# Kernel optimization log

Measured on AMD Instinct MI355X. Metric: run time of the kernel, lower is better.

Reference implementation:

```python
import jax, jax.numpy as jnp
import numpy as np

B, T1, CHUNK = 4, 512, 64
LEFT, RIGHT = 256, 64
T2 = T1 + LEFT + RIGHT          # 832
NPOS = 2 * T1 - 1 + LEFT + RIGHT  # 1343
NFEAT, H, DK = 1024, 16, 64


def setup_inputs() -> dict:
    key = jax.random.key(0)
    ks = jax.random.split(key, 14)
    s = 0.02
    inp = {
        "query":   jax.random.normal(ks[0], (B, T1, NFEAT), jnp.float32),
        "key":     jax.random.normal(ks[1], (B, T2, NFEAT), jnp.float32),
        "value":   jax.random.normal(ks[2], (B, T2, NFEAT), jnp.float32),
        "pos_emb": jax.random.normal(ks[3], (1, NPOS, NFEAT), jnp.float32),
        "Wq":   jax.random.normal(ks[4], (NFEAT, NFEAT), jnp.float32) * s,
        "bq":   jax.random.normal(ks[5], (NFEAT,), jnp.float32) * s,
        "Wk":   jax.random.normal(ks[6], (NFEAT, NFEAT), jnp.float32) * s,
        "bk":   jax.random.normal(ks[7], (NFEAT,), jnp.float32) * s,
        "Wv":   jax.random.normal(ks[8], (NFEAT, NFEAT), jnp.float32) * s,
        "bv":   jax.random.normal(ks[9], (NFEAT,), jnp.float32) * s,
        "Wpos": jax.random.normal(ks[10], (NFEAT, NFEAT), jnp.float32) * s,
        "Wout": jax.random.normal(ks[11], (NFEAT, NFEAT), jnp.float32) * s,
        "bout": jax.random.normal(ks[12], (NFEAT,), jnp.float32) * s,
        "pos_bias_u": jax.random.normal(ks[13], (H, DK), jnp.float32) * s,
        "pos_bias_v": jax.random.normal(jax.random.fold_in(key, 99), (H, DK), jnp.float32) * s,
    }
    # chunk mask with right context: key index j maps to absolute position a = j - LEFT;
    # query i (chunk c = i // CHUNK) may attend a in [c*CHUNK - LEFT, (c+1)*CHUNK + RIGHT)
    c = np.arange(T1) // CHUNK
    a = np.arange(T2) - LEFT
    allowed = (a[None, :] < (c[:, None] + 1) * CHUNK + RIGHT) & (a[None, :] >= c[:, None] * CHUNK - LEFT)
    inp["mask"] = jnp.broadcast_to(jnp.asarray(allowed, dtype=bool)[None], (B, T1, T2))
    inp["left_context_size"] = LEFT
    inp["right_context_size"] = RIGHT
    return inp


def _rel_shift(x, left, right):
    # x: (b, h, t1, 2*t1-1+left+right) -> (b, h, t1, t1+left+right)
    # matches torch as_strided: out[..., i, j] = x[..., i, j - i + t1 - 1]
    b, h, t1, n = x.shape
    t2 = t1 + left + right
    idx = jnp.arange(t2)[None, :] - jnp.arange(t1)[:, None] + (t1 - 1)  # (t1, t2)
    return jnp.take_along_axis(x, idx[None, None], axis=-1)


def reference(query, key, value, pos_emb, mask, Wq, bq, Wk, bk, Wv, bv,
              Wpos, Wout, bout, pos_bias_u, pos_bias_v,
              left_context_size, right_context_size):
    b, t1, _ = query.shape
    q = (query @ Wq.T + bq).reshape(b, t1, H, DK)                       # (b, t1, h, d)
    k = (key @ Wk.T + bk).reshape(b, -1, H, DK).transpose(0, 2, 1, 3)    # (b, h, t2, d)
    v = (value @ Wv.T + bv).reshape(b, -1, H, DK).transpose(0, 2, 1, 3)  # (b, h, t2, d)
    p = (pos_emb @ Wpos.T).reshape(pos_emb.shape[0], -1, H, DK).transpose(0, 2, 1, 3)  # (1, h, n, d)

    q_u = (q + pos_bias_u).transpose(0, 2, 1, 3)   # (b, h, t1, d)
    q_v = (q + pos_bias_v).transpose(0, 2, 1, 3)   # (b, h, t1, d)

    matrix_ac = jnp.einsum('bhqd,bhkd->bhqk', q_u, k)          # (b, h, t1, t2)
    matrix_bd = jnp.einsum('bhqd,ohnd->bhqn', q_v, p)          # (b, h, t1, n)
    matrix_bd = _rel_shift(matrix_bd, left_context_size, right_context_size)

    scores = (matrix_ac + matrix_bd) / jnp.sqrt(jnp.float32(DK))
    m = mask[:, None, :, :]                                    # (b, 1, t1, t2), True = attend
    scores = jnp.where(m, scores, -jnp.inf)
    attn = jax.nn.softmax(scores.astype(jnp.float32), axis=-1).astype(value.dtype)
    attn = jnp.where(m, attn, 0.0)

    x = jnp.einsum('bhqk,bhkd->bqhd', attn, v).reshape(b, t1, H * DK)
    out = x @ Wout.T + bout                                     # (b, t1, n_feat)
    new_cache = jnp.concatenate([k, v], axis=-1)                # (b, h, t2, 2*d)
    return out, new_cache
```

## Files before the change

kernel.cpp:

```cpp
#include <hip/hip_runtime.h>
#include <cstdint>

typedef unsigned short u16;
using short8 = __attribute__((ext_vector_type(8))) short;
using f32x4  = __attribute__((ext_vector_type(4))) float;

#define T1 512
#define T2 832
#define NH 16
#define NPLOC 448

__device__ __forceinline__ u16 f2b(float f){
  union { float f; uint32_t u; } c; c.f = f;
  uint32_t u = c.u;
  u += 0x7fffu + ((u >> 16) & 1u);
  return (u16)(u >> 16);
}
__device__ __forceinline__ float b2f(u16 b){
  union { uint32_t u; float f; } c; c.u = (uint32_t)b << 16; return c.f;
}
__device__ __forceinline__ void async16(const void* g, void* l){
  __builtin_amdgcn_global_load_lds(
      (const __attribute__((address_space(1))) unsigned int*)g,
      (__attribute__((address_space(3))) unsigned int*)l, 16, 0, 0);
}

struct CvtSeg { const float* src; u16* dst; int nblk; };
struct CvtArgs { CvtSeg s[9]; };

__global__ __launch_bounds__(256) void cvt_all(CvtArgs a){
  int rel = blockIdx.x, seg = 0;
  while (rel >= a.s[seg].nblk){ rel -= a.s[seg].nblk; ++seg; }
  int i = rel * 256 + threadIdx.x;
  float4 v = ((const float4*)a.s[seg].src)[i];
  uint64_t p = (uint64_t)f2b(v.x) | ((uint64_t)f2b(v.y) << 16)
             | ((uint64_t)f2b(v.z) << 32) | ((uint64_t)f2b(v.w) << 48);
  *(uint64_t*)(a.s[seg].dst + (size_t)i * 4) = p;
}

__device__ __forceinline__ void gemm_core128(const u16* __restrict__ A, const u16* __restrict__ W,
    int m0, int n0, int tid, f32x4 acc[4][4])
{
  __shared__ __align__(16) u16 As0[4096];
  __shared__ __align__(16) u16 As1[4096];
  __shared__ __align__(16) u16 As2[4096];
  __shared__ __align__(16) u16 Bs0[4096];
  __shared__ __align__(16) u16 Bs1[4096];
  __shared__ __align__(16) u16 Bs2[4096];

  int lane = tid & 63, w = tid >> 6;
  int wr = w >> 1, wc = w & 1;
  const int lr = lane & 15, g = lane >> 4;
  const int sslot = (g ^ ((lr >> 1) & 3)) * 8;

  int r = tid >> 2;
  int ssl = ((tid & 3) ^ ((tid >> 3) & 3)) * 8;
  const u16* Asrc = A + (size_t)(m0 + r) * 1024 + ssl;
  const u16* Bsrc = W + (size_t)(n0 + r) * 1024 + ssl;

  auto stage = [&](int k0, u16* as, u16* bs){
    async16(Asrc + k0,         as + tid*8);
    async16(Asrc + 65536 + k0, as + 2048 + tid*8);
    async16(Bsrc + k0,         bs + tid*8);
    async16(Bsrc + 65536 + k0, bs + 2048 + tid*8);
  };

  auto step = [&](const u16* as, const u16* bs, u16* sas, u16* sbs,
                  int kstage, bool do_stage, bool last){
    if (last) asm volatile("s_waitcnt vmcnt(0)" ::: "memory");
    else      asm volatile("s_waitcnt vmcnt(4)" ::: "memory");
    __builtin_amdgcn_sched_barrier(0);
    __builtin_amdgcn_s_barrier();
    __builtin_amdgcn_sched_barrier(0);
    short8 a[4], b[4];
    #pragma unroll
    for (int m = 0; m < 4; ++m) a[m] = *(const short8*)&as[(wr*64 + m*16 + lr)*32 + sslot];
    #pragma unroll
    for (int n = 0; n < 4; ++n) b[n] = *(const short8*)&bs[(wc*64 + n*16 + lr)*32 + sslot];
    if (do_stage) stage(kstage, sas, sbs);
    __builtin_amdgcn_s_setprio(1);
    #pragma unroll
    for (int m = 0; m < 4; ++m)
      #pragma unroll
      for (int n = 0; n < 4; ++n)
        acc[m][n] = __builtin_amdgcn_mfma_f32_16x16x32_bf16(a[m], b[n], acc[m][n], 0, 0, 0);
    __builtin_amdgcn_s_setprio(0);
    asm volatile("s_waitcnt lgkmcnt(0)" ::: "memory");
    __builtin_amdgcn_sched_barrier(0);
  };

  stage(0,  As0, Bs0);
  stage(32, As1, Bs1);
  for (int s = 0; s < 30; s += 3){
    step(As0, Bs0, As2, Bs2, (s+2)*32, true, false);
    step(As1, Bs1, As0, Bs0, (s+3)*32, true, false);
    step(As2, Bs2, As1, Bs1, (s+4)*32, true, false);
  }
  step(As0, Bs0, As2, Bs2, 0, false, false);
  step(As1, Bs1, As2, Bs2, 0, false, true);
}

__device__ __forceinline__ void gemm_core64(const u16* __restrict__ A, const u16* __restrict__ W,
    int m0, int n0, int tid, f32x4 acc[4][2])
{
  __shared__ __align__(16) u16 As0[2048];
  __shared__ __align__(16) u16 As1[2048];
  __shared__ __align__(16) u16 As2[2048];
  __shared__ __align__(16) u16 Bs0[4096];
  __shared__ __align__(16) u16 Bs1[4096];
  __shared__ __align__(16) u16 Bs2[4096];

  int lane = tid & 63, wc = tid >> 6;
  const int lr = lane & 15, g = lane >> 4;
  const int sslot = (g ^ ((lr >> 1) & 3)) * 8;

  int r = tid >> 2;
  int ssl = ((tid & 3) ^ ((tid >> 3) & 3)) * 8;
  const u16* Asrc = A + (size_t)(m0 + r) * 1024 + ssl;
  const u16* Bsrc = W + (size_t)(n0 + r) * 1024 + ssl;

  auto stage = [&](int k0, u16* as, u16* bs){
    async16(Asrc + k0,         as + tid*8);
    async16(Bsrc + k0,         bs + tid*8);
    async16(Bsrc + 65536 + k0, bs + 2048 + tid*8);
  };

  auto step = [&](const u16* as, const u16* bs, u16* sas, u16* sbs,
                  int kstage, bool do_stage, bool last){
    if (last) asm volatile("s_waitcnt vmcnt(0)" ::: "memory");
    else      asm volatile("s_waitcnt vmcnt(3)" ::: "memory");
    __builtin_amdgcn_sched_barrier(0);
    __builtin_amdgcn_s_barrier();
    __builtin_amdgcn_sched_barrier(0);
    short8 a[4], b[2];
    #pragma unroll
    for (int m = 0; m < 4; ++m) a[m] = *(const short8*)&as[(m*16 + lr)*32 + sslot];
    #pragma unroll
    for (int n = 0; n < 2; ++n) b[n] = *(const short8*)&bs[(wc*32 + n*16 + lr)*32 + sslot];
    if (do_stage) stage(kstage, sas, sbs);
    __builtin_amdgcn_s_setprio(1);
    #pragma unroll
    for (int m = 0; m < 4; ++m)
      #pragma unroll
      for (int n = 0; n < 2; ++n)
        acc[m][n] = __builtin_amdgcn_mfma_f32_16x16x32_bf16(a[m], b[n], acc[m][n], 0, 0, 0);
    __builtin_amdgcn_s_setprio(0);
    asm volatile("s_waitcnt lgkmcnt(0)" ::: "memory");
    __builtin_amdgcn_sched_barrier(0);
  };

  stage(0,  As0, Bs0);
  stage(32, As1, Bs1);
  for (int s = 0; s < 30; s += 3){
    step(As0, Bs0, As2, Bs2, (s+2)*32, true, false);
    step(As1, Bs1, As0, Bs0, (s+3)*32, true, false);
    step(As2, Bs2, As1, Bs1, (s+4)*32, true, false);
  }
  step(As0, Bs0, As2, Bs2, 0, false, false);
  step(As1, Bs1, As2, Bs2, 0, false, true);
}

struct G4Args {
  const u16 *q, *k, *v, *p;
  const u16 *Wq, *Wk, *Wv, *Wp;
  const float *bq, *bk, *bv, *pbu, *pbv;
  u16 *qu, *qv2, *katt, *vatt, *patt;
  float *cache;
};

__global__ __launch_bounds__(256, 3) void gemm4(G4Args ga){
  int bid0 = blockIdx.x;
  int bid = (bid0 & 7) * 72 + (bid0 >> 3);
  int tid = threadIdx.x;
  int mode, mb; const u16 *A, *W;
  if (bid < 128)      { mode = 0; mb = bid >> 3;         A = ga.q; W = ga.Wq; }
  else if (bid < 336) { mode = 1; mb = (bid - 128) >> 3; A = ga.k; W = ga.Wk; }
  else if (bid < 544) { mode = 2; mb = (bid - 336) >> 3; A = ga.v; W = ga.Wv; }
  else                { mode = 3; mb = (bid - 544) >> 3; A = ga.p; W = ga.Wp; }
  int m0 = mb * 128, n0 = (bid & 7) * 128;
  f32x4 acc[4][4] = {};
  gemm_core128(A, W, m0, n0, tid, acc);

  int lane = tid & 63, w = tid >> 6;
  int wr = w >> 1, wc = w & 1;
  const int lr = lane & 15, g = lane >> 4;
  #pragma unroll
  for (int m = 0; m < 4; ++m){
    #pragma unroll
    for (int n = 0; n < 4; ++n){
      #pragma unroll
      for (int j = 0; j < 4; ++j){
        int row = m0 + wr*64 + m*16 + g*4 + j;
        int col = n0 + wc*64 + n*16 + lr;
        float vv = acc[m][n][j];
        if (mode == 0){
          vv += ga.bq[col];
          int h = col >> 6, d = col & 63, b_ = row >> 9, t = row & 511;
          size_t o = ((size_t)((b_*NH + h)*T1 + t))*64 + d;
          ga.qu [o] = f2b(vv + ga.pbu[col]);
          ga.qv2[o] = f2b(vv + ga.pbv[col]);
        } else if (mode == 1 || mode == 2){
          vv += (mode == 1 ? ga.bk : ga.bv)[col];
          int h = col >> 6, d = col & 63;
          int b_ = row / T2, t2 = row - b_*T2;
          size_t base = (size_t)(b_*NH + h)*T2 + t2;
          ga.cache[base*128 + (mode == 2 ? 64 : 0) + d] = vv;
          (mode == 1 ? ga.katt : ga.vatt)[base*64 + d] = f2b(vv);
        } else {
          if (row < NPLOC){
            int h = col >> 6, d = col & 63;
            ga.patt[((size_t)h*NPLOC + row)*64 + d] = f2b(vv);
          }
        }
      }
    }
  }
}

__global__ __launch_bounds__(256, 4) void gemm_out(const u16* __restrict__ A, const u16* __restrict__ W,
                                                   const float* __restrict__ bias, float* __restrict__ out){
  int bid0 = blockIdx.x;
  int bid = (bid0 & 7) * 32 + (bid0 >> 3);
  int m0 = (bid >> 3) * 64, n0 = (bid & 7) * 128;
  int tid = threadIdx.x;
  f32x4 acc[4][2] = {};
  gemm_core64(A, W, m0, n0, tid, acc);
  int lane = tid & 63, wc = tid >> 6;
  const int lr = lane & 15, g = lane >> 4;
  #pragma unroll
  for (int m = 0; m < 4; ++m)
    #pragma unroll
    for (int n = 0; n < 2; ++n)
      #pragma unroll
      for (int j = 0; j < 4; ++j){
        int row = m0 + m*16 + g*4 + j;
        int col = n0 + wc*32 + n*16 + lr;
        out[(size_t)row*1024 + col] = acc[m][n][j] + bias[col];
      }
}

__global__ __launch_bounds__(256, 2) void attn_v2(
    const u16* __restrict__ qu, const u16* __restrict__ qv,
    const u16* __restrict__ katt, const u16* __restrict__ vatt,
    const u16* __restrict__ patt, u16* __restrict__ xout)
{
  __shared__ __align__(16) u16 SB[64*384];
  __shared__ __align__(16) u16 STG[14336];
  int tid = threadIdx.x, lane = tid & 63, w = tid >> 6;
  int bid0 = blockIdx.x;
  int bid = (bid0 & 7) * 64 + (bid0 >> 3);
  int c = bid & 7, h = (bid >> 3) & 15, b = bid >> 7;
  int bh = b*NH + h;
  const int lr = lane & 15, g = lane >> 4, lk = g * 8;

  auto sb_off = [&](int r, int cc) -> uint32_t {
    return ((uint32_t)(r*384 + cc)*2) ^ ((uint32_t)(r & 15) << 4);
  };
  auto stg_swz = [&](uint32_t o) -> uint32_t { return o ^ (((o >> 7) & 7u) << 4); };
  auto vt_off = [&](int d, int kk) -> uint32_t {
    return ((uint32_t)(d*192 + kk)*2) ^ ((uint32_t)(((d & 7) ^ ((d >> 3) & 7))) << 4);
  };

  int qrow = 16*w + lr;
  const u16* qub = qu + ((size_t)bh*T1 + c*64 + qrow)*64;
  const u16* qvb = qv + ((size_t)bh*T1 + c*64 + qrow)*64;
  short8 qu0 = *(const short8*)(qub + lk);
  short8 qu1 = *(const short8*)(qub + 32 + lk);
  short8 qv0 = *(const short8*)(qvb + lk);
  short8 qv1 = *(const short8*)(qvb + 32 + lk);

  const char* psrc = (const char*)(patt + (size_t)h*NPLOC*64);
  for (int pc = 0; pc < 2; ++pc){
    #pragma unroll
    for (int i = 0; i < 7; ++i){
      uint32_t o = (uint32_t)(i*256 + tid)*16;
      async16(psrc + pc*28672 + stg_swz(o), (char*)STG + o);
    }
    __syncthreads();
    for (int nt = 0; nt < 14; ++nt){
      uint32_t bo = (uint32_t)((nt*16 + lr)*64)*2;
      short8 b0 = *(const short8*)((const char*)STG + stg_swz(bo + lk*2));
      short8 b1 = *(const short8*)((const char*)STG + stg_swz(bo + (32 + lk)*2));
      f32x4 acc = {0.f,0.f,0.f,0.f};
      __builtin_amdgcn_s_setprio(1);
      acc = __builtin_amdgcn_mfma_f32_16x16x32_bf16(qv0, b0, acc, 0, 0, 0);
      acc = __builtin_amdgcn_mfma_f32_16x16x32_bf16(qv1, b1, acc, 0, 0, 0);
      __builtin_amdgcn_s_setprio(0);
      int nl = pc*224 + nt*16 + lr;
      #pragma unroll
      for (int j = 0; j < 4; ++j){
        int r = 16*w + g*4 + j;
        int jj = nl + r - 63;
        if (jj >= 0 && jj < 384) *(u16*)((char*)SB + sb_off(r, jj)) = f2b(acc[j]);
      }
    }
    __syncthreads();
  }

  const char* ksrc = (const char*)(katt + ((size_t)bh*T2 + c*64)*64);
  f32x4 accs[24];
  #pragma unroll
  for (int t = 0; t < 24; ++t) accs[t] = (f32x4){0.f,0.f,0.f,0.f};
  #pragma unroll
  for (int kc = 0; kc < 2; ++kc){
    #pragma unroll
    for (int i = 0; i < 6; ++i){
      uint32_t o = (uint32_t)(i*256 + tid)*16;
      async16(ksrc + kc*24576 + stg_swz(o), (char*)STG + o);
    }
    __syncthreads();
    #pragma unroll
    for (int nt = 0; nt < 12; ++nt){
      uint32_t bo = (uint32_t)((nt*16 + lr)*64)*2;
      short8 b0 = *(const short8*)((const char*)STG + stg_swz(bo + lk*2));
      short8 b1 = *(const short8*)((const char*)STG + stg_swz(bo + (32 + lk)*2));
      int t = kc*12 + nt;
      __builtin_amdgcn_s_setprio(1);
      accs[t] = __builtin_amdgcn_mfma_f32_16x16x32_bf16(qu0, b0, accs[t], 0, 0, 0);
      accs[t] = __builtin_amdgcn_mfma_f32_16x16x32_bf16(qu1, b1, accs[t], 0, 0, 0);
      __builtin_amdgcn_s_setprio(0);
    }
    __syncthreads();
  }

  #pragma unroll
  for (int t = 0; t < 24; ++t)
    #pragma unroll
    for (int j = 0; j < 4; ++j){
      int r = 16*w + g*4 + j, cc = t*16 + lr;
      accs[t][j] += b2f(*(const u16*)((const char*)SB + sb_off(r, cc)));
    }
  float mx[4] = {-1e30f,-1e30f,-1e30f,-1e30f};
  #pragma unroll
  for (int t = 0; t < 24; ++t)
    #pragma unroll
    for (int j = 0; j < 4; ++j) mx[j] = fmaxf(mx[j], accs[t][j]);
  #pragma unroll
  for (int j = 0; j < 4; ++j){
    mx[j] = fmaxf(mx[j], __shfl_xor(mx[j], 1));
    mx[j] = fmaxf(mx[j], __shfl_xor(mx[j], 2));
    mx[j] = fmaxf(mx[j], __shfl_xor(mx[j], 4));
    mx[j] = fmaxf(mx[j], __shfl_xor(mx[j], 8));
  }
  float sm[4] = {0.f,0.f,0.f,0.f};
  #pragma unroll
  for (int t = 0; t < 24; ++t)
    #pragma unroll
    for (int j = 0; j < 4; ++j){
      accs[t][j] = __expf((accs[t][j] - mx[j]) * 0.125f);
      sm[j] += accs[t][j];
    }
  #pragma unroll
  for (int j = 0; j < 4; ++j){
    sm[j] += __shfl_xor(sm[j], 1);
    sm[j] += __shfl_xor(sm[j], 2);
    sm[j] += __shfl_xor(sm[j], 4);
    sm[j] += __shfl_xor(sm[j], 8);
    sm[j] = 1.f / sm[j];
  }
  #pragma unroll
  for (int t = 0; t < 24; ++t)
    #pragma unroll
    for (int j = 0; j < 4; ++j){
      int r = 16*w + g*4 + j, cc = t*16 + lr;
      *(u16*)((char*)SB + sb_off(r, cc)) = f2b(accs[t][j] * sm[j]);
    }
  __syncthreads();

  f32x4 acco[4] = {};
  #pragma unroll
  for (int vc = 0; vc < 2; ++vc){
    if (vc) __syncthreads();
    const u16* vb = vatt + ((size_t)bh*T2 + c*64 + vc*192)*64;
    #pragma unroll
    for (int i = 0; i < 6; ++i){
      int e = (i*256 + tid)*8;
      int kk = e >> 6, d0 = e & 63;
      uint4 vv4 = *(const uint4*)(vb + (size_t)kk*64 + d0);
      u16 uu[8] = { (u16)(vv4.x & 0xffff), (u16)(vv4.x >> 16), (u16)(vv4.y & 0xffff), (u16)(vv4.y >> 16),
                    (u16)(vv4.z & 0xffff), (u16)(vv4.z >> 16), (u16)(vv4.w & 0xffff), (u16)(vv4.w >> 16) };
      #pragma unroll
      for (int j = 0; j < 8; ++j)
        *(u16*)((char*)STG + vt_off(d0 + j, kk)) = uu[j];
    }
    __syncthreads();
    #pragma unroll
    for (int kt = 0; kt < 6; ++kt){
      short8 a = *(const short8*)((const char*)SB + sb_off(16*w + lr, vc*192 + kt*32 + lk));
      __builtin_amdgcn_s_setprio(1);
      #pragma unroll
      for (int n = 0; n < 4; ++n){
        short8 bb = *(const short8*)((const char*)STG + vt_off(n*16 + lr, kt*32 + lk));
        acco[n] = __builtin_amdgcn_mfma_f32_16x16x32_bf16(a, bb, acco[n], 0, 0, 0);
      }
      __builtin_amdgcn_s_setprio(0);
    }
  }

  #pragma unroll
  for (int n = 0; n < 4; ++n)
    #pragma unroll
    for (int j = 0; j < 4; ++j){
      int r = 16*w + g*4 + j;
      int t = c*64 + r, d = n*16 + lr;
      xout[((size_t)b*T1 + t)*1024 + h*64 + d] = f2b(acco[n][j]);
    }
}

extern "C" void kernel_launch(void* const* d_in, const int* in_sizes, int n_in,
                              void* d_out, int out_size, void* d_ws, size_t ws_size,
                              hipStream_t stream)
{
  const float* query = (const float*)d_in[0];
  const float* key   = (const float*)d_in[1];
  const float* value = (const float*)d_in[2];
  const float* pos   = (const float*)d_in[3];
  const float* Wq  = (const float*)d_in[4];
  const float* bq  = (const float*)d_in[5];
  const float* Wk  = (const float*)d_in[6];
  const float* bk  = (const float*)d_in[7];
  const float* Wv  = (const float*)d_in[8];
  const float* bv  = (const float*)d_in[9];
  const float* Wp  = (const float*)d_in[10];
  const float* Wo  = (const float*)d_in[11];
  const float* bo  = (const float*)d_in[12];
  const float* pbu = (const float*)d_in[13];
  const float* pbv = (const float*)d_in[14];

  float* out   = (float*)d_out;
  float* cache = out + 2097152;

  u16* ws     = (u16*)d_ws;
  u16* q_bf   = ws;
  u16* key_bf = ws + 2097152;
  u16* val_bf = ws + 5505024;
  u16* pos_bf = ws + 8912896;
  u16* Wq_bf  = ws + 9437184;
  u16* Wk_bf  = ws + 10485760;
  u16* Wv_bf  = ws + 11534336;
  u16* Wp_bf  = ws + 12582912;
  u16* Wo_bf  = ws + 13631488;
  u16* qu_bf  = ws + 14680064;
  u16* qv_bf  = ws + 16777216;
  u16* katt   = ws + 18874368;
  u16* vatt   = ws + 22282240;
  u16* patt   = ws + 25690112;
  u16* x_bf   = ws + 26148864;

  CvtArgs ca;
  ca.s[0] = { query,            q_bf,   2048 };
  ca.s[1] = { key,              key_bf, 3328 };
  ca.s[2] = { value,            val_bf, 3328 };
  ca.s[3] = { Wq,               Wq_bf,  1024 };
  ca.s[4] = { Wk,               Wk_bf,  1024 };
  ca.s[5] = { Wv,               Wv_bf,  1024 };
  ca.s[6] = { Wp,               Wp_bf,  1024 };
  ca.s[7] = { Wo,               Wo_bf,  1024 };
  ca.s[8] = { pos + 448*1024,   pos_bf, 448 };
  cvt_all<<<14272, 256, 0, stream>>>(ca);

  G4Args ga;
  ga.q = q_bf; ga.k = key_bf; ga.v = val_bf; ga.p = pos_bf;
  ga.Wq = Wq_bf; ga.Wk = Wk_bf; ga.Wv = Wv_bf; ga.Wp = Wp_bf;
  ga.bq = bq; ga.bk = bk; ga.bv = bv; ga.pbu = pbu; ga.pbv = pbv;
  ga.qu = qu_bf; ga.qv2 = qv_bf; ga.katt = katt; ga.vatt = vatt; ga.patt = patt;
  ga.cache = cache;
  gemm4<<<576, 256, 0, stream>>>(ga);

  attn_v2<<<512, 256, 0, stream>>>(qu_bf, qv_bf, katt, vatt, patt, x_bf);

  gemm_out<<<256, 256, 0, stream>>>(x_bf, Wo_bf, bo, out);
}
```

Baseline: 92.55 us.

## Double-buffer GEMM staging and pipeline attention loads across phases

The GEMM cores drop from triple to double LDS buffering, with an extra barrier before each refill. This roughly halves shared memory and lets gemm4 raise its launch bound to four blocks per SM. The attention kernel is rewritten as attn_v3 with two 16KB staging buffers. It issues async loads for the next positional, key or value chunk while the current chunk computes, and prefetches V into registers during the softmax. This trades extra barriers and register pressure for overlap of global loads with MFMA work.

```diff
diff --git a/kernel.cpp b/kernel.cpp
--- a/kernel.cpp
+++ b/kernel.cpp
@@ -43,10 +43,8 @@
 {
   __shared__ __align__(16) u16 As0[4096];
   __shared__ __align__(16) u16 As1[4096];
-  __shared__ __align__(16) u16 As2[4096];
   __shared__ __align__(16) u16 Bs0[4096];
   __shared__ __align__(16) u16 Bs1[4096];
-  __shared__ __align__(16) u16 Bs2[4096];
 
   int lane = tid & 63, w = tid >> 6;
   int wr = w >> 1, wc = w & 1;
@@ -65,8 +63,7 @@
     async16(Bsrc + 65536 + k0, bs + 2048 + tid*8);
   };
 
-  auto step = [&](const u16* as, const u16* bs, u16* sas, u16* sbs,
-                  int kstage, bool do_stage, bool last){
+  auto step = [&](u16* as, u16* bs, int kstage, bool do_stage, bool last){
     if (last) asm volatile("s_waitcnt vmcnt(0)" ::: "memory");
     else      asm volatile("s_waitcnt vmcnt(4)" ::: "memory");
     __builtin_amdgcn_sched_barrier(0);
@@ -77,7 +74,12 @@
     for (int m = 0; m < 4; ++m) a[m] = *(const short8*)&as[(wr*64 + m*16 + lr)*32 + sslot];
     #pragma unroll
     for (int n = 0; n < 4; ++n) b[n] = *(const short8*)&bs[(wc*64 + n*16 + lr)*32 + sslot];
-    if (do_stage) stage(kstage, sas, sbs);
+    asm volatile("s_waitcnt lgkmcnt(0)" ::: "memory");
+    __builtin_amdgcn_sched_barrier(0);
+    __builtin_amdgcn_s_barrier();
+    __builtin_amdgcn_sched_barrier(0);
+    if (do_stage) stage(kstage, as, bs);
+    __builtin_amdgcn_sched_barrier(0);
     __builtin_amdgcn_s_setprio(1);
     #pragma unroll
     for (int m = 0; m < 4; ++m)
@@ -85,19 +87,15 @@
       for (int n = 0; n < 4; ++n)
         acc[m][n] = __builtin_amdgcn_mfma_f32_16x16x32_bf16(a[m], b[n], acc[m][n], 0, 0, 0);
     __builtin_amdgcn_s_setprio(0);
-    asm volatile("s_waitcnt lgkmcnt(0)" ::: "memory");
-    __builtin_amdgcn_sched_barrier(0);
   };
 
   stage(0,  As0, Bs0);
   stage(32, As1, Bs1);
-  for (int s = 0; s < 30; s += 3){
-    step(As0, Bs0, As2, Bs2, (s+2)*32, true, false);
-    step(As1, Bs1, As0, Bs0, (s+3)*32, true, false);
-    step(As2, Bs2, As1, Bs1, (s+4)*32, true, false);
+  __builtin_amdgcn_sched_barrier(0);
+  for (int it = 0; it < 16; ++it){
+    step(As0, Bs0, it*64 + 64, it < 15, false);
+    step(As1, Bs1, it*64 + 96, it < 15, it == 15);
   }
-  step(As0, Bs0, As2, Bs2, 0, false, false);
-  step(As1, Bs1, As2, Bs2, 0, false, true);
 }
 
 __device__ __forceinline__ void gemm_core64(const u16* __restrict__ A, const u16* __restrict__ W,
@@ -105,10 +103,8 @@
 {
   __shared__ __align__(16) u16 As0[2048];
   __shared__ __align__(16) u16 As1[2048];
-  __shared__ __align__(16) u16 As2[2048];
   __shared__ __align__(16) u16 Bs0[4096];
   __shared__ __align__(16) u16 Bs1[4096];
-  __shared__ __align__(16) u16 Bs2[4096];
 
   int lane = tid & 63, wc = tid >> 6;
   const int lr = lane & 15, g = lane >> 4;
@@ -125,8 +121,7 @@
     async16(Bsrc + 65536 + k0, bs + 2048 + tid*8);
   };
 
-  auto step = [&](const u16* as, const u16* bs, u16* sas, u16* sbs,
-                  int kstage, bool do_stage, bool last){
+  auto step = [&](u16* as, u16* bs, int kstage, bool do_stage, bool last){
     if (last) asm volatile("s_waitcnt vmcnt(0)" ::: "memory");
     else      asm volatile("s_waitcnt vmcnt(3)" ::: "memory");
     __builtin_amdgcn_sched_barrier(0);
@@ -137,7 +132,12 @@
     for (int m = 0; m < 4; ++m) a[m] = *(const short8*)&as[(m*16 + lr)*32 + sslot];
     #pragma unroll
     for (int n = 0; n < 2; ++n) b[n] = *(const short8*)&bs[(wc*32 + n*16 + lr)*32 + sslot];
-    if (do_stage) stage(kstage, sas, sbs);
+    asm volatile("s_waitcnt lgkmcnt(0)" ::: "memory");
+    __builtin_amdgcn_sched_barrier(0);
+    __builtin_amdgcn_s_barrier();
+    __builtin_amdgcn_sched_barrier(0);
+    if (do_stage) stage(kstage, as, bs);
+    __builtin_amdgcn_sched_barrier(0);
     __builtin_amdgcn_s_setprio(1);
     #pragma unroll
     for (int m = 0; m < 4; ++m)
@@ -145,19 +145,15 @@
       for (int n = 0; n < 2; ++n)
         acc[m][n] = __builtin_amdgcn_mfma_f32_16x16x32_bf16(a[m], b[n], acc[m][n], 0, 0, 0);
     __builtin_amdgcn_s_setprio(0);
-    asm volatile("s_waitcnt lgkmcnt(0)" ::: "memory");
-    __builtin_amdgcn_sched_barrier(0);
   };
 
   stage(0,  As0, Bs0);
   stage(32, As1, Bs1);
-  for (int s = 0; s < 30; s += 3){
-    step(As0, Bs0, As2, Bs2, (s+2)*32, true, false);
-    step(As1, Bs1, As0, Bs0, (s+3)*32, true, false);
-    step(As2, Bs2, As1, Bs1, (s+4)*32, true, false);
+  __builtin_amdgcn_sched_barrier(0);
+  for (int it = 0; it < 16; ++it){
+    step(As0, Bs0, it*64 + 64, it < 15, false);
+    step(As1, Bs1, it*64 + 96, it < 15, it == 15);
   }
-  step(As0, Bs0, As2, Bs2, 0, false, false);
-  step(As1, Bs1, As2, Bs2, 0, false, true);
 }
 
 struct G4Args {
@@ -168,7 +164,7 @@
   float *cache;
 };
 
-__global__ __launch_bounds__(256, 3) void gemm4(G4Args ga){
+__global__ __launch_bounds__(256, 4) void gemm4(G4Args ga){
   int bid0 = blockIdx.x;
   int bid = (bid0 & 7) * 72 + (bid0 >> 3);
   int tid = threadIdx.x;
@@ -239,13 +235,32 @@
       }
 }
 
-__global__ __launch_bounds__(256, 2) void attn_v2(
+#define PHASE_HEAD(N) \
+  asm volatile("s_waitcnt vmcnt(" #N ")" ::: "memory"); \
+  __builtin_amdgcn_sched_barrier(0); \
+  __builtin_amdgcn_s_barrier(); \
+  __builtin_amdgcn_sched_barrier(0);
+
+#define PHASE_TAIL \
+  __builtin_amdgcn_sched_barrier(0); \
+  __builtin_amdgcn_s_barrier(); \
+  __builtin_amdgcn_sched_barrier(0);
+
+#define VT_TAIL \
+  asm volatile("s_waitcnt lgkmcnt(0)" ::: "memory"); \
+  __builtin_amdgcn_sched_barrier(0); \
+  __builtin_amdgcn_s_barrier(); \
+  __builtin_amdgcn_sched_barrier(0);
+
+__global__ __launch_bounds__(256, 2) void attn_v3(
     const u16* __restrict__ qu, const u16* __restrict__ qv,
     const u16* __restrict__ katt, const u16* __restrict__ vatt,
     const u16* __restrict__ patt, u16* __restrict__ xout)
 {
   __shared__ __align__(16) u16 SB[64*384];
-  __shared__ __align__(16) u16 STG[14336];
+  __shared__ __align__(16) u16 S0[8192];
+  __shared__ __align__(16) u16 S1[8192];
+
   int tid = threadIdx.x, lane = tid & 63, w = tid >> 6;
   int bid0 = blockIdx.x;
   int bid = (bid0 & 7) * 64 + (bid0 >> 3);
@@ -258,7 +273,7 @@
   };
   auto stg_swz = [&](uint32_t o) -> uint32_t { return o ^ (((o >> 7) & 7u) << 4); };
   auto vt_off = [&](int d, int kk) -> uint32_t {
-    return ((uint32_t)(d*192 + kk)*2) ^ ((uint32_t)(((d & 7) ^ ((d >> 3) & 7))) << 4);
+    return ((uint32_t)(d*128 + kk)*2) ^ ((uint32_t)(((d & 7) ^ ((d >> 3) & 7))) << 4);
   };
 
   int qrow = 16*w + lr;
@@ -268,60 +283,102 @@
   short8 qu1 = *(const short8*)(qub + 32 + lk);
   short8 qv0 = *(const short8*)(qvb + lk);
   short8 qv1 = *(const short8*)(qvb + 32 + lk);
+  __builtin_amdgcn_sched_barrier(0);
 
   const char* psrc = (const char*)(patt + (size_t)h*NPLOC*64);
-  for (int pc = 0; pc < 2; ++pc){
-    #pragma unroll
-    for (int i = 0; i < 7; ++i){
+  const char* ksrc = (const char*)(katt + ((size_t)bh*T2 + c*64)*64);
+  const u16*  vsrc = vatt + ((size_t)bh*T2 + c*64)*64;
+
+  auto issue4 = [&](const char* src, u16* dst){
+    #pragma unroll
+    for (int i = 0; i < 4; ++i){
       uint32_t o = (uint32_t)(i*256 + tid)*16;
-      async16(psrc + pc*28672 + stg_swz(o), (char*)STG + o);
-    }
-    __syncthreads();
-    for (int nt = 0; nt < 14; ++nt){
-      uint32_t bo = (uint32_t)((nt*16 + lr)*64)*2;
-      short8 b0 = *(const short8*)((const char*)STG + stg_swz(bo + lk*2));
-      short8 b1 = *(const short8*)((const char*)STG + stg_swz(bo + (32 + lk)*2));
-      f32x4 acc = {0.f,0.f,0.f,0.f};
-      __builtin_amdgcn_s_setprio(1);
-      acc = __builtin_amdgcn_mfma_f32_16x16x32_bf16(qv0, b0, acc, 0, 0, 0);
-      acc = __builtin_amdgcn_mfma_f32_16x16x32_bf16(qv1, b1, acc, 0, 0, 0);
-      __builtin_amdgcn_s_setprio(0);
-      int nl = pc*224 + nt*16 + lr;
+      async16(src + stg_swz(o), (char*)dst + o);
+    }
+  };
+
+  uint4 vstg0, vstg1, vstg2, vstg3;
+  auto vload = [&](int vc){
+    const u16* vb = vsrc + vc*8192;
+    vstg0 = *(const uint4*)(vb + (0*256 + tid)*8);
+    vstg1 = *(const uint4*)(vb + (1*256 + tid)*8);
+    vstg2 = *(const uint4*)(vb + (2*256 + tid)*8);
+    vstg3 = *(const uint4*)(vb + (3*256 + tid)*8);
+  };
+  auto vtwrite = [&](u16* sbuf){
+    #pragma unroll
+    for (int i = 0; i < 4; ++i){
+      uint4 vv4 = (i == 0) ? vstg0 : (i == 1) ? vstg1 : (i == 2) ? vstg2 : vstg3;
+      int e = (i*256 + tid)*8;
+      int kk = e >> 6, d0 = e & 63;
+      u16 uu[8] = { (u16)(vv4.x & 0xffff), (u16)(vv4.x >> 16), (u16)(vv4.y & 0xffff), (u16)(vv4.y >> 16),
+                    (u16)(vv4.z & 0xffff), (u16)(vv4.z >> 16), (u16)(vv4.w & 0xffff), (u16)(vv4.w >> 16) };
       #pragma unroll
-      for (int j = 0; j < 4; ++j){
-        int r = 16*w + g*4 + j;
-        int jj = nl + r - 63;
-        if (jj >= 0 && jj < 384) *(u16*)((char*)SB + sb_off(r, jj)) = f2b(acc[j]);
-      }
-    }
-    __syncthreads();
-  }
-
-  const char* ksrc = (const char*)(katt + ((size_t)bh*T2 + c*64)*64);
+      for (int j = 0; j < 8; ++j)
+        *(u16*)((char*)sbuf + vt_off(d0 + j, kk)) = uu[j];
+    }
+  };
+
+  #define BD_CHUNK(PC, SBUF) \
+    _Pragma("unroll") \
+    for (int nt = 0; nt < 8; ++nt){ \
+      uint32_t bo = (uint32_t)((nt*16 + lr)*64)*2; \
+      short8 b0 = *(const short8*)((const char*)SBUF + stg_swz(bo + lk*2)); \
+      short8 b1 = *(const short8*)((const char*)SBUF + stg_swz(bo + (32 + lk)*2)); \
+      f32x4 acc = {0.f,0.f,0.f,0.f}; \
+      __builtin_amdgcn_s_setprio(1); \
+      acc = __builtin_amdgcn_mfma_f32_16x16x32_bf16(qv0, b0, acc, 0, 0, 0); \
+      acc = __builtin_amdgcn_mfma_f32_16x16x32_bf16(qv1, b1, acc, 0, 0, 0); \
+      __builtin_amdgcn_s_setprio(0); \
+      int nl = (PC)*128 + nt*16 + lr; \
+      _Pragma("unroll") \
+      for (int j = 0; j < 4; ++j){ \
+        int r = 16*w + g*4 + j; \
+        int jj = nl + r - 63; \
+        if (jj >= 0 && jj < 384) *(u16*)((char*)SB + sb_off(r, jj)) = f2b(acc[j]); \
+      } \
+    }
+
+  #define AC_CHUNK(KC, SBUF) \
+    _Pragma("unroll") \
+    for (int nt = 0; nt < 8; ++nt){ \
+      uint32_t bo = (uint32_t)((nt*16 + lr)*64)*2; \
+      short8 b0 = *(const short8*)((const char*)SBUF + stg_swz(bo + lk*2)); \
+      short8 b1 = *(const short8*)((const char*)SBUF + stg_swz(bo + (32 + lk)*2)); \
+      __builtin_amdgcn_s_setprio(1); \
+      accs[(KC)*8 + nt] = __builtin_amdgcn_mfma_f32_16x16x32_bf16(qu0, b0, accs[(KC)*8 + nt], 0, 0, 0); \
+      accs[(KC)*8 + nt] = __builtin_amdgcn_mfma_f32_16x16x32_bf16(qu1, b1, accs[(KC)*8 + nt], 0, 0, 0); \
+      __builtin_amdgcn_s_setprio(0); \
+    }
+
+  #define PV_CHUNK(VC, SBUF) \
+    _Pragma("unroll") \
+    for (int kt = 0; kt < 4; ++kt){ \
+      short8 a = *(const short8*)((const char*)SB + sb_off(16*w + lr, (VC)*128 + kt*32 + lk)); \
+      __builtin_amdgcn_s_setprio(1); \
+      _Pragma("unroll") \
+      for (int n = 0; n < 4; ++n){ \
+        short8 bb = *(const short8*)((const char*)SBUF + vt_off(n*16 + lr, kt*32 + lk)); \
+        acco[n] = __builtin_amdgcn_mfma_f32_16x16x32_bf16(a, bb, acco[n], 0, 0, 0); \
+      } \
+      __builtin_amdgcn_s_setprio(0); \
+    }
+
   f32x4 accs[24];
   #pragma unroll
   for (int t = 0; t < 24; ++t) accs[t] = (f32x4){0.f,0.f,0.f,0.f};
-  #pragma unroll
-  for (int kc = 0; kc < 2; ++kc){
-    #pragma unroll
-    for (int i = 0; i < 6; ++i){
-      uint32_t o = (uint32_t)(i*256 + tid)*16;
-      async16(ksrc + kc*24576 + stg_swz(o), (char*)STG + o);
-    }
-    __syncthreads();
-    #pragma unroll
-    for (int nt = 0; nt < 12; ++nt){
-      uint32_t bo = (uint32_t)((nt*16 + lr)*64)*2;
-      short8 b0 = *(const short8*)((const char*)STG + stg_swz(bo + lk*2));
-      short8 b1 = *(const short8*)((const char*)STG + stg_swz(bo + (32 + lk)*2));
-      int t = kc*12 + nt;
-      __builtin_amdgcn_s_setprio(1);
-      accs[t] = __builtin_amdgcn_mfma_f32_16x16x32_bf16(qu0, b0, accs[t], 0, 0, 0);
-      accs[t] = __builtin_amdgcn_mfma_f32_16x16x32_bf16(qu1, b1, accs[t], 0, 0, 0);
-      __builtin_amdgcn_s_setprio(0);
-    }
-    __syncthreads();
-  }
+  f32x4 acco[4] = {};
+
+  issue4(psrc,          S0);
+  issue4(psrc + 16384,  S1);
+
+  PHASE_HEAD(4) BD_CHUNK(0, S0) PHASE_TAIL issue4(psrc + 32768, S0);
+  PHASE_HEAD(4) BD_CHUNK(1, S1) PHASE_TAIL issue4(psrc + 49152, S1);
+  PHASE_HEAD(4) BD_CHUNK(2, S0) PHASE_TAIL issue4(ksrc,         S0);
+  PHASE_HEAD(4) BD_CHUNK(3, S1) PHASE_TAIL issue4(ksrc + 16384, S1);
+  PHASE_HEAD(4) AC_CHUNK(0, S0) PHASE_TAIL issue4(ksrc + 32768, S0);
+  PHASE_HEAD(4) AC_CHUNK(1, S1) PHASE_TAIL vload(0);
+  PHASE_HEAD(4) AC_CHUNK(2, S0)
 
   #pragma unroll
   for (int t = 0; t < 24; ++t)
@@ -365,37 +422,27 @@
       int r = 16*w + g*4 + j, cc = t*16 + lr;
       *(u16*)((char*)SB + sb_off(r, cc)) = f2b(accs[t][j] * sm[j]);
     }
-  __syncthreads();
-
-  f32x4 acco[4] = {};
-  #pragma unroll
-  for (int vc = 0; vc < 2; ++vc){
-    if (vc) __syncthreads();
-    const u16* vb = vatt + ((size_t)bh*T2 + c*64 + vc*192)*64;
-    #pragma unroll
-    for (int i = 0; i < 6; ++i){
-      int e = (i*256 + tid)*8;
-      int kk = e >> 6, d0 = e & 63;
-      uint4 vv4 = *(const uint4*)(vb + (size_t)kk*64 + d0);
-      u16 uu[8] = { (u16)(vv4.x & 0xffff), (u16)(vv4.x >> 16), (u16)(vv4.y & 0xffff), (u16)(vv4.y >> 16),
-                    (u16)(vv4.z & 0xffff), (u16)(vv4.z >> 16), (u16)(vv4.w & 0xffff), (u16)(vv4.w >> 16) };
-      #pragma unroll
-      for (int j = 0; j < 8; ++j)
-        *(u16*)((char*)STG + vt_off(d0 + j, kk)) = uu[j];
-    }
-    __syncthreads();
-    #pragma unroll
-    for (int kt = 0; kt < 6; ++kt){
-      short8 a = *(const short8*)((const char*)SB + sb_off(16*w + lr, vc*192 + kt*32 + lk));
-      __builtin_amdgcn_s_setprio(1);
-      #pragma unroll
-      for (int n = 0; n < 4; ++n){
-        short8 bb = *(const short8*)((const char*)STG + vt_off(n*16 + lr, kt*32 + lk));
-        acco[n] = __builtin_amdgcn_mfma_f32_16x16x32_bf16(a, bb, acco[n], 0, 0, 0);
-      }
-      __builtin_amdgcn_s_setprio(0);
-    }
-  }
+
+  asm volatile("s_waitcnt vmcnt(0)" ::: "memory");
+  __builtin_amdgcn_sched_barrier(0);
+  vtwrite(S1);
+  vload(1);
+  VT_TAIL
+
+  PV_CHUNK(0, S1)
+  asm volatile("s_waitcnt vmcnt(0)" ::: "memory");
+  __builtin_amdgcn_sched_barrier(0);
+  vtwrite(S0);
+  vload(2);
+  VT_TAIL
+
+  PV_CHUNK(1, S0)
+  asm volatile("s_waitcnt vmcnt(0)" ::: "memory");
+  __builtin_amdgcn_sched_barrier(0);
+  vtwrite(S1);
+  VT_TAIL
+
+  PV_CHUNK(2, S1)
 
   #pragma unroll
   for (int n = 0; n < 4; ++n)
@@ -467,7 +514,7 @@
   ga.cache = cache;
   gemm4<<<576, 256, 0, stream>>>(ga);
 
-  attn_v2<<<512, 256, 0, stream>>>(qu_bf, qv_bf, katt, vatt, patt, x_bf);
+  attn_v3<<<512, 256, 0, stream>>>(qu_bf, qv_bf, katt, vatt, patt, x_bf);
 
   gemm_out<<<256, 256, 0, stream>>>(x_bf, Wo_bf, bo, out);
 }
```

After: 89.84 us. 2.9% less time.
